# Kernel tuning notes

Measured on AMD Instinct MI355X. Metric: run time of the kernel, lower is better.

## Reference

```python
import jax, jax.numpy as jnp
import numpy as np

C_IN = 128
C_INNER = 128


def setup_inputs() -> dict:
    key = jax.random.key(0)
    ks = jax.random.split(key, 9)
    b, c, h, w = 4, C_IN, 64, 64
    s = 1.0 / np.sqrt(c)
    x = jax.random.normal(ks[0], (b, c, h, w), dtype=jnp.float32)
    Wq = jax.random.normal(ks[1], (C_INNER, C_IN), dtype=jnp.float32) * s
    bq = jnp.zeros((C_INNER,), dtype=jnp.float32)
    Wk = jax.random.normal(ks[2], (C_INNER, C_IN), dtype=jnp.float32) * s
    bk = jnp.zeros((C_INNER,), dtype=jnp.float32)
    Wv = jax.random.normal(ks[3], (C_INNER, C_IN), dtype=jnp.float32) * s
    bv = jnp.zeros((C_INNER,), dtype=jnp.float32)
    Wo = jax.random.normal(ks[4], (C_IN, C_INNER), dtype=jnp.float32) * (1.0 / np.sqrt(C_INNER))
    bo = jnp.zeros((C_IN,), dtype=jnp.float32)
    return {"x": x, "Wq": Wq, "bq": bq, "Wk": Wk, "bk": bk,
            "Wv": Wv, "bv": bv, "Wo": Wo, "bo": bo}


def _conv1x1(x, W, bias):
    # x: (b,c,h,w), W: (o,c) -> (b,o,h,w)
    return jnp.einsum('oc,bchw->bohw', W, x) + bias[None, :, None, None]


def reference(x, Wq, bq, Wk, bk, Wv, bv, Wo, bo):
    b, c, h, w = x.shape
    ci = Wq.shape[0]
    n = h * w
    q = _conv1x1(x, Wq, bq).reshape(b, ci, n)          # (b, ci, n)
    k = _conv1x1(x, Wk, bk).reshape(b, ci, n)          # (b, ci, n)
    v = _conv1x1(x, Wv, bv).reshape(b, ci, n)          # (b, ci, n)
    # attn = softmax(q^T @ k) over keys
    attn = jnp.einsum('bci,bcj->bij', q, k)            # (b, n, n)
    attn = jax.nn.softmax(attn, axis=-1)
    out = jnp.einsum('bij,bcj->bci', attn, v)          # (b, ci, n)
    out = out.reshape(b, ci, h, w)
    out = _conv1x1(out, Wo, bo)
    return out + x
```

## Files before the change

### kernel.cpp

```cpp
#include <hip/hip_runtime.h>
#include <math.h>
#include <stdint.h>

#define CDIM 128
#define NTOT 4096

typedef _Float16 f16x8 __attribute__((ext_vector_type(8)));
typedef float floatx4 __attribute__((ext_vector_type(4)));

static __device__ __forceinline__ floatx4 mfma16(f16x8 a, f16x8 b, floatx4 c) {
    return __builtin_amdgcn_mfma_f32_16x16x32_f16(a, b, c, 0, 0, 0);
}
static __device__ __forceinline__ unsigned short f2h(float f) {
    _Float16 h = (_Float16)f;
    return __builtin_bit_cast(unsigned short, h);
}
static __device__ __forceinline__ float h2f(unsigned short u) {
    return (float)__builtin_bit_cast(_Float16, u);
}

#define SWZ(row, cc) ((((row) << 7)) + ((((cc) ^ ((row) & 15))) << 3))

__global__ __launch_bounds__(256) void qkv_proj_kernel(
    const float* __restrict__ x,
    const float* __restrict__ Wq, const float* __restrict__ bq,
    const float* __restrict__ Wk, const float* __restrict__ bk,
    const float* __restrict__ Wv, const float* __restrict__ bv,
    unsigned short* __restrict__ qo, unsigned short* __restrict__ ko,
    unsigned short* __restrict__ vo)
{
    __shared__ __align__(16) unsigned short Xs[64][136];
    __shared__ __align__(16) unsigned short Ws[64][136];

    const int t = threadIdx.x, b = blockIdx.y, n0 = blockIdx.x * 64;
    const int zo = blockIdx.z * 64;
    const int w = t >> 6, quad = (t >> 4) & 3, l15 = t & 15;

    {
        const int n = (t & 15) * 4;
        const int c = (t >> 4) * 8;
        float4 xr[8];
        #pragma unroll
        for (int j = 0; j < 8; ++j)
            xr[j] = *(const float4*)&x[((size_t)b * CDIM + c + j) * NTOT + n0 + n];
        #pragma unroll
        for (int k = 0; k < 4; ++k) {
            ushort4 ulo, uhi;
            ulo.x = f2h(((const float*)&xr[0])[k]);
            ulo.y = f2h(((const float*)&xr[1])[k]);
            ulo.z = f2h(((const float*)&xr[2])[k]);
            ulo.w = f2h(((const float*)&xr[3])[k]);
            uhi.x = f2h(((const float*)&xr[4])[k]);
            uhi.y = f2h(((const float*)&xr[5])[k]);
            uhi.z = f2h(((const float*)&xr[6])[k]);
            uhi.w = f2h(((const float*)&xr[7])[k]);
            *(ushort4*)&Xs[n + k][c]     = ulo;
            *(ushort4*)&Xs[n + k][c + 4] = uhi;
        }
    }

    f16x8 xf[4];
    for (int s = 0; s < 3; ++s) {
        const float* W    = (s == 0) ? Wq : (s == 1) ? Wk : Wv;
        const float* bias = (s == 0) ? bq : (s == 1) ? bk : bv;
        if (s) __syncthreads();
        {
            int o = t >> 2, ch = (t & 3) * 32;
            #pragma unroll
            for (int i = 0; i < 8; ++i) {
                float4 f4 = *(const float4*)&W[(size_t)(zo + o) * CDIM + ch + i * 4];
                ushort4 u = { f2h(f4.x), f2h(f4.y), f2h(f4.z), f2h(f4.w) };
                *(ushort4*)&Ws[o][ch + i * 4] = u;
            }
        }
        __syncthreads();
        if (s == 0) {
            #pragma unroll
            for (int f = 0; f < 4; ++f)
                xf[f] = *(const f16x8*)&Xs[w * 16 + l15][f * 32 + quad * 8];
        }

        if (s < 2) {
            unsigned short* dst = (s == 0) ? qo : ko;
            #pragma unroll
            for (int ot = 0; ot < 4; ++ot) {
                floatx4 acc = (floatx4){0.f, 0.f, 0.f, 0.f};
                #pragma unroll
                for (int f = 0; f < 4; ++f) {
                    f16x8 aW = *(const f16x8*)&Ws[ot * 16 + l15][f * 32 + quad * 8];
                    acc = mfma16(aW, xf[f], acc);
                }
                const int ob = zo + ot * 16 + quad * 4;
                ushort4 u;
                u.x = f2h(acc[0] + bias[ob + 0]);
                u.y = f2h(acc[1] + bias[ob + 1]);
                u.z = f2h(acc[2] + bias[ob + 2]);
                u.w = f2h(acc[3] + bias[ob + 3]);
                *(ushort4*)&dst[((size_t)b * NTOT + n0 + w * 16 + l15) * CDIM + ob] = u;
            }
        } else {
            #pragma unroll
            for (int ot = 0; ot < 4; ++ot) {
                floatx4 acc = (floatx4){0.f, 0.f, 0.f, 0.f};
                #pragma unroll
                for (int f = 0; f < 4; ++f) {
                    f16x8 bW = *(const f16x8*)&Ws[ot * 16 + l15][f * 32 + quad * 8];
                    acc = mfma16(xf[f], bW, acc);
                }
                const int o = zo + ot * 16 + l15;
                const float bv_ = bias[o];
                ushort4 u;
                u.x = f2h(acc[0] + bv_); u.y = f2h(acc[1] + bv_);
                u.z = f2h(acc[2] + bv_); u.w = f2h(acc[3] + bv_);
                *(ushort4*)&vo[((size_t)b * CDIM + o) * NTOT + n0 + w * 16 + quad * 4] = u;
            }
        }
    }
}

__global__ __launch_bounds__(256, 2) void attn_kernel(
    const unsigned short* __restrict__ qg,
    const unsigned short* __restrict__ kg,
    const unsigned short* __restrict__ vg,
    unsigned short* __restrict__ Op,
    float* __restrict__ Ms, float* __restrict__ Ls)
{
    __shared__ __align__(16) unsigned short Ks[128 * 128];
    __shared__ __align__(16) unsigned short Vs[128 * 128];

    const int t = threadIdx.x;
    const int w = t >> 6, quad = (t >> 4) & 3, l15 = t & 15;
    const int b = blockIdx.y;
    const int z = blockIdx.z;
    const int i0 = blockIdx.x * 128;
    const int jbase = z * 1024;
    const size_t vbase = (size_t)b * CDIM * NTOT;

    f16x8 bQ[2][4];
    #pragma unroll
    for (int nt = 0; nt < 2; ++nt) {
        const size_t qrow = ((size_t)b * NTOT + i0 + w * 32 + nt * 16 + l15) * CDIM;
        #pragma unroll
        for (int f = 0; f < 4; ++f)
            bQ[nt][f] = *(const f16x8*)&qg[qrow + f * 32 + quad * 8];
    }

    floatx4 accO[2][8];
    #pragma unroll
    for (int nt = 0; nt < 2; ++nt)
        #pragma unroll
        for (int dt = 0; dt < 8; ++dt) accO[nt][dt] = (floatx4){0.f, 0.f, 0.f, 0.f};
    float m_run[2] = {-INFINITY, -INFINITY};
    float l_part[2] = {0.f, 0.f};

    for (int iter = 0; iter < 8; ++iter) {
        const int j0 = jbase + iter * 128;
        __syncthreads();

        {
            const size_t kb_ = ((size_t)b * NTOT + j0) * CDIM;
            #pragma unroll
            for (int r = 0; r < 8; ++r) {
                int flat = r * 256 + t;
                int row = flat >> 4, cc = flat & 15;
                *(uint4*)&Ks[SWZ(row, cc)] =
                    *(const uint4*)&kg[kb_ + (size_t)row * CDIM + cc * 8];
                *(uint4*)&Vs[SWZ(row, cc)] =
                    *(const uint4*)&vg[vbase + (size_t)row * NTOT + j0 + cc * 8];
            }
        }
        __syncthreads();

        floatx4 accT[2][8];
        #pragma unroll
        for (int nt = 0; nt < 2; ++nt)
            #pragma unroll
            for (int jt = 0; jt < 8; ++jt) accT[nt][jt] = (floatx4){0.f, 0.f, 0.f, 0.f};
        #pragma unroll
        for (int jt = 0; jt < 8; ++jt)
            #pragma unroll
            for (int f = 0; f < 4; ++f) {
                f16x8 aK = *(const f16x8*)&Ks[SWZ(jt * 16 + l15, f * 4 + quad)];
                accT[0][jt] = mfma16(aK, bQ[0][f], accT[0][jt]);
                accT[1][jt] = mfma16(aK, bQ[1][f], accT[1][jt]);
            }

        float m_new[2], alpha[2];
        ushort4 pu[2][8];
        #pragma unroll
        for (int nt = 0; nt < 2; ++nt) {
            float tm = accT[nt][0][0];
            #pragma unroll
            for (int jt = 0; jt < 8; ++jt)
                #pragma unroll
                for (int r = 0; r < 4; ++r) tm = fmaxf(tm, accT[nt][jt][r]);
            tm = fmaxf(tm, __shfl_xor(tm, 16));
            tm = fmaxf(tm, __shfl_xor(tm, 32));
            m_new[nt] = fmaxf(m_run[nt], tm);
            alpha[nt] = __expf(m_run[nt] - m_new[nt]);
            m_run[nt] = m_new[nt];
            float ps = 0.f;
            #pragma unroll
            for (int jt = 0; jt < 8; ++jt) {
                float p0 = __expf(accT[nt][jt][0] - m_new[nt]);
                float p1 = __expf(accT[nt][jt][1] - m_new[nt]);
                float p2 = __expf(accT[nt][jt][2] - m_new[nt]);
                float p3 = __expf(accT[nt][jt][3] - m_new[nt]);
                ps += (p0 + p1) + (p2 + p3);
                pu[nt][jt].x = f2h(p0); pu[nt][jt].y = f2h(p1);
                pu[nt][jt].z = f2h(p2); pu[nt][jt].w = f2h(p3);
            }
            l_part[nt] = l_part[nt] * alpha[nt] + ps;
            #pragma unroll
            for (int dt = 0; dt < 8; ++dt) {
                accO[nt][dt][0] *= alpha[nt]; accO[nt][dt][1] *= alpha[nt];
                accO[nt][dt][2] *= alpha[nt]; accO[nt][dt][3] *= alpha[nt];
            }
        }

        __syncthreads();

        #pragma unroll
        for (int nt = 0; nt < 2; ++nt) {
            const int prow = w * 32 + nt * 16 + l15;
            #pragma unroll
            for (int jt = 0; jt < 8; ++jt)
                *(ushort4*)&Ks[SWZ(prow, 2 * jt + (quad >> 1)) + (quad & 1) * 4] =
                    pu[nt][jt];
        }

        f16x8 bP[2][4];
        #pragma unroll
        for (int nt = 0; nt < 2; ++nt) {
            const int prow = w * 32 + nt * 16 + l15;
            #pragma unroll
            for (int kb = 0; kb < 4; ++kb)
                bP[nt][kb] = *(const f16x8*)&Ks[SWZ(prow, kb * 4 + quad)];
        }
        #pragma unroll
        for (int dt = 0; dt < 8; ++dt)
            #pragma unroll
            for (int kb = 0; kb < 4; ++kb) {
                f16x8 aV = *(const f16x8*)&Vs[SWZ(dt * 16 + l15, kb * 4 + quad)];
                accO[0][dt] = mfma16(aV, bP[0][kb], accO[0][dt]);
                accO[1][dt] = mfma16(aV, bP[1][kb], accO[1][dt]);
            }
    }

    #pragma unroll
    for (int nt = 0; nt < 2; ++nt) {
        float lf = l_part[nt];
        lf += __shfl_xor(lf, 16);
        lf += __shfl_xor(lf, 32);
        const float inv = 1.0f / lf;
        const size_t orow =
            (((size_t)z * 4 + b) * NTOT + i0 + w * 32 + nt * 16 + l15) * CDIM;
        #pragma unroll
        for (int dt = 0; dt < 8; ++dt) {
            ushort4 u;
            u.x = f2h(accO[nt][dt][0] * inv); u.y = f2h(accO[nt][dt][1] * inv);
            u.z = f2h(accO[nt][dt][2] * inv); u.w = f2h(accO[nt][dt][3] * inv);
            *(ushort4*)&Op[orow + dt * 16 + quad * 4] = u;
        }
        if (quad == 0) {
            const int idx = (z * 4 + b) * NTOT + i0 + w * 32 + nt * 16 + l15;
            Ms[idx] = m_run[nt];
            Ls[idx] = lf;
        }
    }
}

__global__ __launch_bounds__(256) void out_proj_kernel(
    const unsigned short* __restrict__ Op,
    const float* __restrict__ Ms, const float* __restrict__ Ls,
    const float* __restrict__ Wo, const float* __restrict__ bo,
    const float* __restrict__ x, float* __restrict__ out)
{
    __shared__ __align__(16) unsigned short As[64][136];
    __shared__ __align__(16) unsigned short Ws[64][136];

    const int t = threadIdx.x, b = blockIdx.y, n0 = blockIdx.x * 64;
    const int zo = blockIdx.z * 64;
    const int w = t >> 6, quad = (t >> 4) & 3, l15 = t & 15;

    const size_t PER = (size_t)NTOT * 4 * CDIM;

    #pragma unroll
    for (int r = 0; r < 4; ++r) {
        int flat = r * 256 + t;
        int row = flat >> 4, c16 = (flat & 15) * 8;
        const int bn = b * NTOT + n0 + row;
        float m0 = Ms[bn], m1 = Ms[bn + 16384], m2 = Ms[bn + 32768], m3 = Ms[bn + 49152];
        float M = fmaxf(fmaxf(m0, m1), fmaxf(m2, m3));
        float w0 = Ls[bn]         * __expf(m0 - M);
        float w1 = Ls[bn + 16384] * __expf(m1 - M);
        float w2 = Ls[bn + 32768] * __expf(m2 - M);
        float w3 = Ls[bn + 49152] * __expf(m3 - M);
        const float inv = 1.0f / (w0 + w1 + w2 + w3);
        w0 *= inv; w1 *= inv; w2 *= inv; w3 *= inv;

        const size_t base = (size_t)bn * CDIM + c16;
        uint4 a0 = *(const uint4*)&Op[base];
        uint4 a1 = *(const uint4*)&Op[PER + base];
        uint4 a2 = *(const uint4*)&Op[2 * PER + base];
        uint4 a3 = *(const uint4*)&Op[3 * PER + base];
        const unsigned short* p0 = (const unsigned short*)&a0;
        const unsigned short* p1 = (const unsigned short*)&a1;
        const unsigned short* p2 = (const unsigned short*)&a2;
        const unsigned short* p3 = (const unsigned short*)&a3;
        unsigned short mv[8];
        #pragma unroll
        for (int j = 0; j < 8; ++j)
            mv[j] = f2h(w0 * h2f(p0[j]) + w1 * h2f(p1[j]) +
                        w2 * h2f(p2[j]) + w3 * h2f(p3[j]));
        *(uint4*)&As[row][c16] = *(const uint4*)mv;
    }
    {
        int o = t >> 2, ch = (t & 3) * 32;
        #pragma unroll
        for (int i = 0; i < 8; ++i) {
            float4 f4 = *(const float4*)&Wo[(size_t)(zo + o) * CDIM + ch + i * 4];
            ushort4 u = { f2h(f4.x), f2h(f4.y), f2h(f4.z), f2h(f4.w) };
            *(ushort4*)&Ws[o][ch + i * 4] = u;
        }
    }
    __syncthreads();

    f16x8 bA[4];
    #pragma unroll
    for (int f = 0; f < 4; ++f)
        bA[f] = *(const f16x8*)&As[w * 16 + l15][f * 32 + quad * 8];

    #pragma unroll
    for (int ot = 0; ot < 4; ++ot) {
        floatx4 acc = (floatx4){0.f, 0.f, 0.f, 0.f};
        #pragma unroll
        for (int f = 0; f < 4; ++f) {
            f16x8 aW = *(const f16x8*)&Ws[ot * 16 + l15][f * 32 + quad * 8];
            acc = mfma16(aW, bA[f], acc);
        }
        const int ob = zo + ot * 16 + quad * 4;
        #pragma unroll
        for (int r = 0; r < 4; ++r) {
            size_t idx = ((size_t)b * CDIM + ob + r) * NTOT + n0 + w * 16 + l15;
            out[idx] = acc[r] + bo[ob + r] + x[idx];
        }
    }
}

extern "C" void kernel_launch(void* const* d_in, const int* in_sizes, int n_in,
                              void* d_out, int out_size, void* d_ws, size_t ws_size,
                              hipStream_t stream)
{
    const float* x  = (const float*)d_in[0];
    const float* Wq = (const float*)d_in[1];
    const float* bq = (const float*)d_in[2];
    const float* Wk = (const float*)d_in[3];
    const float* bk = (const float*)d_in[4];
    const float* Wv = (const float*)d_in[5];
    const float* bv = (const float*)d_in[6];
    const float* Wo = (const float*)d_in[7];
    const float* bo = (const float*)d_in[8];
    float* out = (float*)d_out;

    const size_t PER = (size_t)4 * CDIM * NTOT;
    unsigned short* q_ws  = (unsigned short*)d_ws;
    unsigned short* k_ws  = q_ws + PER;
    unsigned short* v_ws  = k_ws + PER;
    unsigned short* op_ws = v_ws + PER;
    float*          ms_ws = (float*)(op_ws + 4 * PER);
    float*          ls_ws = ms_ws + 4 * 16384;

    qkv_proj_kernel<<<dim3(64, 4, 2), dim3(256), 0, stream>>>(
        x, Wq, bq, Wk, bk, Wv, bv, q_ws, k_ws, v_ws);
    attn_kernel<<<dim3(32, 4, 4), dim3(256), 0, stream>>>(
        q_ws, k_ws, v_ws, op_ws, ms_ws, ls_ws);
    out_proj_kernel<<<dim3(64, 4, 2), dim3(256), 0, stream>>>(
        op_ws, ms_ws, ls_ws, Wo, bo, x, out);
}
```

Before: 166.9 us.

## Split attention keys eight ways with smaller tiles and exp2-based softmax

The attention kernel now tiles keys in blocks of 64 and splits the key range across 8 z-blocks instead of 4. This halves shared memory per block and raises the occupancy hint to 4, so the grid has twice as many blocks to fill the GPU. Q is pre-scaled by log2(e) in the projection so the softmax can use exp2f, and P is packed with cvt_pkrtz. The output projection merges 8 partial results instead of 4, which adds workspace traffic and reduction work.

```diff
diff --git a/kernel.cpp b/kernel.cpp
--- a/kernel.cpp
+++ b/kernel.cpp
@@ -4,6 +4,7 @@
 
 #define CDIM 128
 #define NTOT 4096
+#define LOG2E 1.4426950408889634f
 
 typedef _Float16 f16x8 __attribute__((ext_vector_type(8)));
 typedef float floatx4 __attribute__((ext_vector_type(4)));
@@ -18,8 +19,14 @@
 static __device__ __forceinline__ float h2f(unsigned short u) {
     return (float)__builtin_bit_cast(_Float16, u);
 }
-
-#define SWZ(row, cc) ((((row) << 7)) + ((((cc) ^ ((row) & 15))) << 3))
+static __device__ __forceinline__ unsigned int pkrtz(float a, float b) {
+    typedef __fp16 hv2 __attribute__((ext_vector_type(2)));
+    hv2 h = __builtin_amdgcn_cvt_pkrtz(a, b);
+    return __builtin_bit_cast(unsigned int, h);
+}
+
+#define SWZK(row, cc) (((row) << 7) + ((((cc) ^ ((row) & 15))) << 3))
+#define SWZV(row, cc) (((row) << 6) + ((((cc) ^ ((row) & 7))) << 3))
 
 __global__ __launch_bounds__(256) void qkv_proj_kernel(
     const float* __restrict__ x,
@@ -63,13 +70,15 @@
     for (int s = 0; s < 3; ++s) {
         const float* W    = (s == 0) ? Wq : (s == 1) ? Wk : Wv;
         const float* bias = (s == 0) ? bq : (s == 1) ? bk : bv;
+        const float wscale = (s == 0) ? LOG2E : 1.0f;
         if (s) __syncthreads();
         {
             int o = t >> 2, ch = (t & 3) * 32;
             #pragma unroll
             for (int i = 0; i < 8; ++i) {
                 float4 f4 = *(const float4*)&W[(size_t)(zo + o) * CDIM + ch + i * 4];
-                ushort4 u = { f2h(f4.x), f2h(f4.y), f2h(f4.z), f2h(f4.w) };
+                ushort4 u = { f2h(f4.x * wscale), f2h(f4.y * wscale),
+                              f2h(f4.z * wscale), f2h(f4.w * wscale) };
                 *(ushort4*)&Ws[o][ch + i * 4] = u;
             }
         }
@@ -92,10 +101,10 @@
                 }
                 const int ob = zo + ot * 16 + quad * 4;
                 ushort4 u;
-                u.x = f2h(acc[0] + bias[ob + 0]);
-                u.y = f2h(acc[1] + bias[ob + 1]);
-                u.z = f2h(acc[2] + bias[ob + 2]);
-                u.w = f2h(acc[3] + bias[ob + 3]);
+                u.x = f2h(acc[0] + wscale * bias[ob + 0]);
+                u.y = f2h(acc[1] + wscale * bias[ob + 1]);
+                u.z = f2h(acc[2] + wscale * bias[ob + 2]);
+                u.w = f2h(acc[3] + wscale * bias[ob + 3]);
                 *(ushort4*)&dst[((size_t)b * NTOT + n0 + w * 16 + l15) * CDIM + ob] = u;
             }
         } else {
@@ -118,22 +127,22 @@
     }
 }
 
-__global__ __launch_bounds__(256, 2) void attn_kernel(
+__global__ __launch_bounds__(256, 4) void attn_kernel(
     const unsigned short* __restrict__ qg,
     const unsigned short* __restrict__ kg,
     const unsigned short* __restrict__ vg,
     unsigned short* __restrict__ Op,
     float* __restrict__ Ms, float* __restrict__ Ls)
 {
-    __shared__ __align__(16) unsigned short Ks[128 * 128];
-    __shared__ __align__(16) unsigned short Vs[128 * 128];
+    __shared__ __align__(16) unsigned short Ks[64 * 128];
+    __shared__ __align__(16) unsigned short Vs[128 * 64];
 
     const int t = threadIdx.x;
     const int w = t >> 6, quad = (t >> 4) & 3, l15 = t & 15;
     const int b = blockIdx.y;
     const int z = blockIdx.z;
     const int i0 = blockIdx.x * 128;
-    const int jbase = z * 1024;
+    const int jbase = z * 512;
     const size_t vbase = (size_t)b * CDIM * NTOT;
 
     f16x8 bQ[2][4];
@@ -154,67 +163,67 @@
     float l_part[2] = {0.f, 0.f};
 
     for (int iter = 0; iter < 8; ++iter) {
-        const int j0 = jbase + iter * 128;
+        const int j0 = jbase + iter * 64;
         __syncthreads();
 
         {
             const size_t kb_ = ((size_t)b * NTOT + j0) * CDIM;
             #pragma unroll
-            for (int r = 0; r < 8; ++r) {
-                int flat = r * 256 + t;
-                int row = flat >> 4, cc = flat & 15;
-                *(uint4*)&Ks[SWZ(row, cc)] =
-                    *(const uint4*)&kg[kb_ + (size_t)row * CDIM + cc * 8];
-                *(uint4*)&Vs[SWZ(row, cc)] =
-                    *(const uint4*)&vg[vbase + (size_t)row * NTOT + j0 + cc * 8];
+            for (int r = 0; r < 4; ++r) {
+                int fk = r * 256 + t;
+                int krow = fk >> 4, kcc = fk & 15;
+                *(uint4*)&Ks[SWZK(krow, kcc)] =
+                    *(const uint4*)&kg[kb_ + (size_t)krow * CDIM + kcc * 8];
+                int vrow = fk >> 3, vcc = fk & 7;
+                *(uint4*)&Vs[SWZV(vrow, vcc)] =
+                    *(const uint4*)&vg[vbase + (size_t)vrow * NTOT + j0 + vcc * 8];
             }
         }
         __syncthreads();
 
-        floatx4 accT[2][8];
+        floatx4 accT[2][4];
         #pragma unroll
         for (int nt = 0; nt < 2; ++nt)
             #pragma unroll
-            for (int jt = 0; jt < 8; ++jt) accT[nt][jt] = (floatx4){0.f, 0.f, 0.f, 0.f};
-        #pragma unroll
-        for (int jt = 0; jt < 8; ++jt)
+            for (int jt = 0; jt < 4; ++jt) accT[nt][jt] = (floatx4){0.f, 0.f, 0.f, 0.f};
+        #pragma unroll
+        for (int jt = 0; jt < 4; ++jt)
             #pragma unroll
             for (int f = 0; f < 4; ++f) {
-                f16x8 aK = *(const f16x8*)&Ks[SWZ(jt * 16 + l15, f * 4 + quad)];
+                f16x8 aK = *(const f16x8*)&Ks[SWZK(jt * 16 + l15, f * 4 + quad)];
                 accT[0][jt] = mfma16(aK, bQ[0][f], accT[0][jt]);
                 accT[1][jt] = mfma16(aK, bQ[1][f], accT[1][jt]);
             }
 
-        float m_new[2], alpha[2];
-        ushort4 pu[2][8];
+        uint2 pu[2][4];
         #pragma unroll
         for (int nt = 0; nt < 2; ++nt) {
             float tm = accT[nt][0][0];
             #pragma unroll
-            for (int jt = 0; jt < 8; ++jt)
+            for (int jt = 0; jt < 4; ++jt)
                 #pragma unroll
                 for (int r = 0; r < 4; ++r) tm = fmaxf(tm, accT[nt][jt][r]);
             tm = fmaxf(tm, __shfl_xor(tm, 16));
             tm = fmaxf(tm, __shfl_xor(tm, 32));
-            m_new[nt] = fmaxf(m_run[nt], tm);
-            alpha[nt] = __expf(m_run[nt] - m_new[nt]);
-            m_run[nt] = m_new[nt];
+            const float m_new = fmaxf(m_run[nt], tm);
+            const float alpha = exp2f(m_run[nt] - m_new);
+            m_run[nt] = m_new;
             float ps = 0.f;
             #pragma unroll
-            for (int jt = 0; jt < 8; ++jt) {
-                float p0 = __expf(accT[nt][jt][0] - m_new[nt]);
-                float p1 = __expf(accT[nt][jt][1] - m_new[nt]);
-                float p2 = __expf(accT[nt][jt][2] - m_new[nt]);
-                float p3 = __expf(accT[nt][jt][3] - m_new[nt]);
+            for (int jt = 0; jt < 4; ++jt) {
+                float p0 = exp2f(accT[nt][jt][0] - m_new);
+                float p1 = exp2f(accT[nt][jt][1] - m_new);
+                float p2 = exp2f(accT[nt][jt][2] - m_new);
+                float p3 = exp2f(accT[nt][jt][3] - m_new);
                 ps += (p0 + p1) + (p2 + p3);
-                pu[nt][jt].x = f2h(p0); pu[nt][jt].y = f2h(p1);
-                pu[nt][jt].z = f2h(p2); pu[nt][jt].w = f2h(p3);
-            }
-            l_part[nt] = l_part[nt] * alpha[nt] + ps;
+                pu[nt][jt].x = pkrtz(p0, p1);
+                pu[nt][jt].y = pkrtz(p2, p3);
+            }
+            l_part[nt] = l_part[nt] * alpha + ps;
             #pragma unroll
             for (int dt = 0; dt < 8; ++dt) {
-                accO[nt][dt][0] *= alpha[nt]; accO[nt][dt][1] *= alpha[nt];
-                accO[nt][dt][2] *= alpha[nt]; accO[nt][dt][3] *= alpha[nt];
+                accO[nt][dt][0] *= alpha; accO[nt][dt][1] *= alpha;
+                accO[nt][dt][2] *= alpha; accO[nt][dt][3] *= alpha;
             }
         }
 
@@ -224,24 +233,24 @@
         for (int nt = 0; nt < 2; ++nt) {
             const int prow = w * 32 + nt * 16 + l15;
             #pragma unroll
-            for (int jt = 0; jt < 8; ++jt)
-                *(ushort4*)&Ks[SWZ(prow, 2 * jt + (quad >> 1)) + (quad & 1) * 4] =
+            for (int jt = 0; jt < 4; ++jt)
+                *(uint2*)&Ks[SWZV(prow, 2 * jt + (quad >> 1)) + (quad & 1) * 4] =
                     pu[nt][jt];
         }
 
-        f16x8 bP[2][4];
+        f16x8 bP[2][2];
         #pragma unroll
         for (int nt = 0; nt < 2; ++nt) {
             const int prow = w * 32 + nt * 16 + l15;
             #pragma unroll
-            for (int kb = 0; kb < 4; ++kb)
-                bP[nt][kb] = *(const f16x8*)&Ks[SWZ(prow, kb * 4 + quad)];
+            for (int kb = 0; kb < 2; ++kb)
+                bP[nt][kb] = *(const f16x8*)&Ks[SWZV(prow, kb * 4 + quad)];
         }
         #pragma unroll
         for (int dt = 0; dt < 8; ++dt)
             #pragma unroll
-            for (int kb = 0; kb < 4; ++kb) {
-                f16x8 aV = *(const f16x8*)&Vs[SWZ(dt * 16 + l15, kb * 4 + quad)];
+            for (int kb = 0; kb < 2; ++kb) {
+                f16x8 aV = *(const f16x8*)&Vs[SWZV(dt * 16 + l15, kb * 4 + quad)];
                 accO[0][dt] = mfma16(aV, bP[0][kb], accO[0][dt]);
                 accO[1][dt] = mfma16(aV, bP[1][kb], accO[1][dt]);
             }
@@ -283,36 +292,37 @@
     const int zo = blockIdx.z * 64;
     const int w = t >> 6, quad = (t >> 4) & 3, l15 = t & 15;
 
-    const size_t PER = (size_t)NTOT * 4 * CDIM;
+    const size_t PER_OP = (size_t)NTOT * 4 * CDIM;
 
     #pragma unroll
     for (int r = 0; r < 4; ++r) {
         int flat = r * 256 + t;
         int row = flat >> 4, c16 = (flat & 15) * 8;
         const int bn = b * NTOT + n0 + row;
-        float m0 = Ms[bn], m1 = Ms[bn + 16384], m2 = Ms[bn + 32768], m3 = Ms[bn + 49152];
-        float M = fmaxf(fmaxf(m0, m1), fmaxf(m2, m3));
-        float w0 = Ls[bn]         * __expf(m0 - M);
-        float w1 = Ls[bn + 16384] * __expf(m1 - M);
-        float w2 = Ls[bn + 32768] * __expf(m2 - M);
-        float w3 = Ls[bn + 49152] * __expf(m3 - M);
-        const float inv = 1.0f / (w0 + w1 + w2 + w3);
-        w0 *= inv; w1 *= inv; w2 *= inv; w3 *= inv;
-
+        float mz[8], wz[8];
+        float M = -INFINITY;
+        #pragma unroll
+        for (int zi = 0; zi < 8; ++zi) { mz[zi] = Ms[bn + zi * 16384]; M = fmaxf(M, mz[zi]); }
+        float wsum = 0.f;
+        #pragma unroll
+        for (int zi = 0; zi < 8; ++zi) {
+            wz[zi] = Ls[bn + zi * 16384] * exp2f(mz[zi] - M);
+            wsum += wz[zi];
+        }
+        const float inv = 1.0f / wsum;
+
+        float sacc[8] = {0.f, 0.f, 0.f, 0.f, 0.f, 0.f, 0.f, 0.f};
         const size_t base = (size_t)bn * CDIM + c16;
-        uint4 a0 = *(const uint4*)&Op[base];
-        uint4 a1 = *(const uint4*)&Op[PER + base];
-        uint4 a2 = *(const uint4*)&Op[2 * PER + base];
-        uint4 a3 = *(const uint4*)&Op[3 * PER + base];
-        const unsigned short* p0 = (const unsigned short*)&a0;
-        const unsigned short* p1 = (const unsigned short*)&a1;
-        const unsigned short* p2 = (const unsigned short*)&a2;
-        const unsigned short* p3 = (const unsigned short*)&a3;
+        #pragma unroll
+        for (int zi = 0; zi < 8; ++zi) {
+            uint4 a = *(const uint4*)&Op[zi * PER_OP + base];
+            const unsigned short* pa = (const unsigned short*)&a;
+            #pragma unroll
+            for (int j = 0; j < 8; ++j) sacc[j] += wz[zi] * h2f(pa[j]);
+        }
         unsigned short mv[8];
         #pragma unroll
-        for (int j = 0; j < 8; ++j)
-            mv[j] = f2h(w0 * h2f(p0[j]) + w1 * h2f(p1[j]) +
-                        w2 * h2f(p2[j]) + w3 * h2f(p3[j]));
+        for (int j = 0; j < 8; ++j) mv[j] = f2h(sacc[j] * inv);
         *(uint4*)&As[row][c16] = *(const uint4*)mv;
     }
     {
@@ -368,12 +378,12 @@
     unsigned short* k_ws  = q_ws + PER;
     unsigned short* v_ws  = k_ws + PER;
     unsigned short* op_ws = v_ws + PER;
-    float*          ms_ws = (float*)(op_ws + 4 * PER);
-    float*          ls_ws = ms_ws + 4 * 16384;
+    float*          ms_ws = (float*)(op_ws + 8 * PER);
+    float*          ls_ws = ms_ws + 8 * 16384;
 
     qkv_proj_kernel<<<dim3(64, 4, 2), dim3(256), 0, stream>>>(
         x, Wq, bq, Wk, bk, Wv, bv, q_ws, k_ws, v_ws);
-    attn_kernel<<<dim3(32, 4, 4), dim3(256), 0, stream>>>(
+    attn_kernel<<<dim3(32, 4, 8), dim3(256), 0, stream>>>(
         q_ws, k_ws, v_ws, op_ws, ms_ws, ls_ws);
     out_proj_kernel<<<dim3(64, 4, 2), dim3(256), 0, stream>>>(
         op_ws, ms_ws, ls_ws, Wo, bo, x, out);
```

After: 272.2 us. +63.1%, slower.
